# Performance work log

Measured on AMD Instinct MI355X. Metric: run time of the kernel, lower is better.

Reference implementation:

```python
import jax, jax.numpy as jnp
import numpy as np

N_NODES = 50000
N_HEDGES = 10000
NNZ_INC = 400000
NNZ_E = 80000
NNZ_V = 400000
VDIM = 128
EDIM = 128
OUT_VDIM = 128
OUT_EDIM = 128


def _spmm(rows, cols, vals, X, n_rows):
    # sparse COO [n_rows, n_cols] @ X  -> [n_rows, d]
    return jax.ops.segment_sum(vals[:, None] * X[cols], rows, num_segments=n_rows)


def setup_inputs() -> dict:
    key = jax.random.key(0)
    ks = jax.random.split(key, 20)
    inp = {
        "vfeat": jax.random.normal(ks[0], (N_NODES, VDIM), jnp.float32),
        "efeat": jax.random.normal(ks[1], (N_HEDGES, EDIM), jnp.float32),
        "invDV": jax.random.uniform(ks[2], (N_NODES,), jnp.float32),
        "invDE": jax.random.uniform(ks[3], (N_HEDGES,), jnp.float32),
        "inc_src": jax.random.randint(ks[4], (NNZ_INC,), 0, N_NODES, jnp.int32),
        "inc_dst": jax.random.randint(ks[5], (NNZ_INC,), 0, N_HEDGES, jnp.int32),
        "emat_rows": jax.random.randint(ks[6], (NNZ_E,), 0, N_HEDGES, jnp.int32),
        "emat_cols": jax.random.randint(ks[7], (NNZ_E,), 0, N_HEDGES, jnp.int32),
        "emat_vals": jax.random.normal(ks[8], (NNZ_E,), jnp.float32),
        "vmat_rows": jax.random.randint(ks[9], (NNZ_V,), 0, N_NODES, jnp.int32),
        "vmat_cols": jax.random.randint(ks[10], (NNZ_V,), 0, N_NODES, jnp.int32),
        "vmat_vals": jax.random.normal(ks[11], (NNZ_V,), jnp.float32),
        # parameters (torch Linear: y = x @ W.T + b)
        "Wv": jax.random.normal(ks[12], (OUT_VDIM, VDIM), jnp.float32) * 0.05,
        "We": jax.random.normal(ks[13], (OUT_EDIM, EDIM), jnp.float32) * 0.05,
        "psi1_W": jax.random.normal(ks[14], (VDIM, VDIM + EDIM), jnp.float32) * 0.05,
        "psi1_b": jnp.zeros((VDIM,), jnp.float32),
        "psi2_W": jax.random.normal(ks[15], (EDIM, OUT_VDIM + EDIM), jnp.float32) * 0.05,
        "psi2_b": jnp.zeros((EDIM,), jnp.float32),
    }
    return inp


def reference(vfeat, efeat, invDV, invDE, inc_src, inc_dst,
              emat_rows, emat_cols, emat_vals,
              vmat_rows, vmat_cols, vmat_vals,
              Wv, We, psi1_W, psi1_b, psi2_W, psi2_b):
    N = vfeat.shape[0]
    E = efeat.shape[0]
    # --- 'in' update_all with psi1: per-incidence concat -> linear -> *invDV[src] -> sum into hyperedge
    x = jnp.concatenate([vfeat[inc_src], efeat[inc_dst]], axis=1)  # [nnz, VDIM+EDIM]
    x = x @ psi1_W.T + psi1_b                                       # [nnz, VDIM]
    x = x * invDV[inc_src][:, None]
    A = jax.ops.segment_sum(x, inc_dst, num_segments=E)             # [E, VDIM]
    A = _spmm(emat_rows, emat_cols, emat_vals, A, E)
    _efeat = A + efeat
    # --- 'con' update_all: node gathers sum of incident hyperedge feats
    _vfeat = jax.ops.segment_sum(_efeat[inc_dst], inc_src, num_segments=N)
    vfeat_out = jax.nn.relu(_vfeat @ Wv.T)                           # [N, OUT_VDIM]
    # --- 'in' update_all with psi2 (dv = ones)
    x2 = jnp.concatenate([vfeat_out[inc_src], efeat[inc_dst]], axis=1)
    x2 = x2 @ psi2_W.T + psi2_b                                      # [nnz, EDIM]
    B = jax.ops.segment_sum(x2, inc_dst, num_segments=E) * invDE[:, None]
    # --- 'con' pass with efeat, then vMat spmm, then 'in' sum back to hyperedges
    _vfeat2 = jax.ops.segment_sum(efeat[inc_dst], inc_src, num_segments=N)
    _vfeat2 = _spmm(vmat_rows, vmat_cols, vmat_vals, _vfeat2, N)
    _efeat2 = jax.ops.segment_sum(_vfeat2[inc_src], inc_dst, num_segments=E)
    _efeat2 = _efeat2 + B
    efeat_out = jax.nn.relu(_efeat2 @ We.T)                          # [E, OUT_EDIM]
    return vfeat_out, efeat_out
```

## Files before the change

kernel.cpp:

```cpp
#include <hip/hip_runtime.h>

#define NN 50000
#define NE 10000
#define NNZ_INC 400000
#define NNZ_E 80000
#define NNZ_V 400000
#define D 128
#define KC 32

#define CAP_D 112
#define CAP_S 40
#define CAP_E 40
#define CAP_V 40

#define CSTR 16

#define GN_ 782
#define GE_ 157
#define G_HINC ((NNZ_INC + 255) / 256)
#define G_EV ((NNZ_E + NNZ_V + 255) / 256)
#define G_CVTN 6250
#define G_CVTE 1250
#define G_NR16 (NN / 16)
#define G_ER16 (NE / 16)

typedef unsigned short u16;
typedef unsigned int u32;

__device__ __forceinline__ u16 f2bf(float x) {
    unsigned u = __float_as_uint(x);
    unsigned r = u + 0x7fffu + ((u >> 16) & 1u);
    return (u16)(r >> 16);
}
__device__ __forceinline__ float bf2f(u16 h) {
    return __uint_as_float(((unsigned)h) << 16);
}

__device__ __forceinline__ void acc8(uint4 u, float acc[8]) {
    acc[0] += __uint_as_float(u.x << 16);
    acc[1] += __uint_as_float(u.x & 0xffff0000u);
    acc[2] += __uint_as_float(u.y << 16);
    acc[3] += __uint_as_float(u.y & 0xffff0000u);
    acc[4] += __uint_as_float(u.z << 16);
    acc[5] += __uint_as_float(u.z & 0xffff0000u);
    acc[6] += __uint_as_float(u.w << 16);
    acc[7] += __uint_as_float(u.w & 0xffff0000u);
}
__device__ __forceinline__ void fma8(uint4 u, float v, float acc[8]) {
    acc[0] = fmaf(v, __uint_as_float(u.x << 16), acc[0]);
    acc[1] = fmaf(v, __uint_as_float(u.x & 0xffff0000u), acc[1]);
    acc[2] = fmaf(v, __uint_as_float(u.y << 16), acc[2]);
    acc[3] = fmaf(v, __uint_as_float(u.y & 0xffff0000u), acc[3]);
    acc[4] = fmaf(v, __uint_as_float(u.z << 16), acc[4]);
    acc[5] = fmaf(v, __uint_as_float(u.z & 0xffff0000u), acc[5]);
    acc[6] = fmaf(v, __uint_as_float(u.w << 16), acc[6]);
    acc[7] = fmaf(v, __uint_as_float(u.w & 0xffff0000u), acc[7]);
}
__device__ __forceinline__ uint4 pack_bf8(const float acc[8]) {
    uint4 o;
    o.x = (u32)f2bf(acc[0]) | ((u32)f2bf(acc[1]) << 16);
    o.y = (u32)f2bf(acc[2]) | ((u32)f2bf(acc[3]) << 16);
    o.z = (u32)f2bf(acc[4]) | ((u32)f2bf(acc[5]) << 16);
    o.w = (u32)f2bf(acc[6]) | ((u32)f2bf(acc[7]) << 16);
    return o;
}

__device__ __forceinline__ void gemm_acc(
    int bx, const float* __restrict__ X, const float* __restrict__ W, int ldw,
    int M, float acc[8][4])
{
    __shared__ float XsT[KC][68];
    __shared__ float Ws[KC][132];
    const int tid = threadIdx.x;
    const int tx = tid & 31, ty = tid >> 5;
    const int row0 = bx * 64;
    const int c0 = tx * 4;
    const int r0 = ty * 8;

#pragma unroll
    for (int r = 0; r < 8; ++r)
#pragma unroll
        for (int c = 0; c < 4; ++c) acc[r][c] = 0.f;

    for (int kc = 0; kc < D; kc += KC) {
        __syncthreads();
#pragma unroll
        for (int it = 0; it < 2; ++it) {
            int l = tid + it * 256;
            int r = l >> 3, k4 = l & 7;
            float4 v = make_float4(0.f, 0.f, 0.f, 0.f);
            int row = row0 + r;
            if (row < M) v = ((const float4*)(X + (size_t)row * D + kc))[k4];
            int k = k4 * 4;
            XsT[k + 0][r] = v.x; XsT[k + 1][r] = v.y;
            XsT[k + 2][r] = v.z; XsT[k + 3][r] = v.w;
        }
#pragma unroll
        for (int it = 0; it < 4; ++it) {
            int l = tid + it * 256;
            int o = l >> 3, k4 = l & 7;
            float4 w = ((const float4*)(W + (size_t)o * ldw + kc))[k4];
            int k = k4 * 4;
            Ws[k + 0][o] = w.x; Ws[k + 1][o] = w.y;
            Ws[k + 2][o] = w.z; Ws[k + 3][o] = w.w;
        }
        __syncthreads();
#pragma unroll
        for (int k = 0; k < KC; ++k) {
            const float4 a0 = *(const float4*)&XsT[k][r0];
            const float4 a1 = *(const float4*)&XsT[k][r0 + 4];
            const float4 b  = *(const float4*)&Ws[k][c0];
            float av[8] = {a0.x, a0.y, a0.z, a0.w, a1.x, a1.y, a1.z, a1.w};
            float bv[4] = {b.x, b.y, b.z, b.w};
#pragma unroll
            for (int r = 0; r < 8; ++r)
#pragma unroll
                for (int c = 0; c < 4; ++c)
                    acc[r][c] = fmaf(av[r], bv[c], acc[r][c]);
        }
    }
}

__global__ __launch_bounds__(256) void mega0(
    const int* __restrict__ inc_src, const int* __restrict__ inc_dst,
    int* __restrict__ cnt_dst, int* __restrict__ cnt_src,
    u16* __restrict__ ell_d, u16* __restrict__ ell_s,
    const float* __restrict__ efeat, const float* __restrict__ vfeat,
    const float* __restrict__ invDV,
    const float* __restrict__ psi1_W, const float* __restrict__ psi1_b, float* __restrict__ PeP,
    const float* __restrict__ psi2_W, const float* __restrict__ psi2_b, float* __restrict__ QeP,
    u16* __restrict__ vfi_b, u16* __restrict__ efeat_b)
{
    int b = blockIdx.x;
    if (b < G_HINC) {
        int i = b * 256 + threadIdx.x;
        if (i < NNZ_INC) {
            int s = inc_src[i], d = inc_dst[i];
            int rd = atomicAdd(cnt_dst + (size_t)d * CSTR, 1);
            if (rd < CAP_D) ell_d[d * CAP_D + rd] = (u16)s;
            int rs = atomicAdd(cnt_src + (size_t)s * CSTR, 1);
            if (rs < CAP_S) ell_s[s * CAP_S + rs] = (u16)d;
        }
    } else if (b < G_HINC + 2 * GE_) {
        int lb = b - G_HINC;
        const float* Wp = (lb < GE_) ? psi1_W + D : psi2_W + D;
        const float* bp = (lb < GE_) ? psi1_b : psi2_b;
        float* outp     = (lb < GE_) ? PeP : QeP;
        int bx = (lb < GE_) ? lb : lb - GE_;
        float acc[8][4];
        gemm_acc(bx, efeat, Wp, 2 * D, NE, acc);
        int tx = threadIdx.x & 31, ty = threadIdx.x >> 5;
        float4 b4 = ((const float4*)bp)[tx];
#pragma unroll
        for (int r = 0; r < 8; ++r) {
            int row = bx * 64 + ty * 8 + r;
            if (row < NE) {
                float4 v = make_float4(acc[r][0] + b4.x, acc[r][1] + b4.y,
                                       acc[r][2] + b4.z, acc[r][3] + b4.w);
                ((float4*)(outp + (size_t)row * D))[tx] = v;
            }
        }
    } else if (b < G_HINC + 2 * GE_ + G_CVTN) {
        int i = ((b - G_HINC - 2 * GE_) * 256 + threadIdx.x) * 4;
        int row = i >> 7;
        float s = invDV[row];
        float4 v = *(const float4*)(vfeat + i);
        ushort4 u;
        u.x = f2bf(v.x * s); u.y = f2bf(v.y * s);
        u.z = f2bf(v.z * s); u.w = f2bf(v.w * s);
        *(ushort4*)(vfi_b + i) = u;
    } else {
        int i = ((b - G_HINC - 2 * GE_ - G_CVTN) * 256 + threadIdx.x) * 4;
        float4 v = *(const float4*)(efeat + i);
        ushort4 u;
        u.x = f2bf(v.x); u.y = f2bf(v.y); u.z = f2bf(v.z); u.w = f2bf(v.w);
        *(ushort4*)(efeat_b + i) = u;
    }
}

__device__ __forceinline__ void segsum_bf_ell16(int rb,
    const int* __restrict__ cnt, int cap, const u16* __restrict__ ell,
    const u16* __restrict__ Tb, u16* __restrict__ Yb, int R)
{
    int r = rb * 16 + (threadIdx.x >> 4);
    int q = threadIdx.x & 15;
    if (r >= R) return;
    int m = min(cnt[(size_t)r * CSTR], cap);
    const u16* lst = ell + (size_t)r * cap;
    float acc[8] = {0.f, 0.f, 0.f, 0.f, 0.f, 0.f, 0.f, 0.f};
    int j = 0;
    for (; j + 3 < m; j += 4) {
        ushort4 ix = *(const ushort4*)(lst + j);
        uint4 u0 = *(const uint4*)(Tb + (size_t)ix.x * D + q * 8);
        uint4 u1 = *(const uint4*)(Tb + (size_t)ix.y * D + q * 8);
        uint4 u2 = *(const uint4*)(Tb + (size_t)ix.z * D + q * 8);
        uint4 u3 = *(const uint4*)(Tb + (size_t)ix.w * D + q * 8);
        acc8(u0, acc); acc8(u1, acc); acc8(u2, acc); acc8(u3, acc);
    }
    for (; j < m; ++j) {
        uint4 u0 = *(const uint4*)(Tb + (size_t)lst[j] * D + q * 8);
        acc8(u0, acc);
    }
    ((uint4*)(Yb + (size_t)r * D))[q] = pack_bf8(acc);
}

__device__ __forceinline__ void segsum_f_ell16(int rb,
    const int* __restrict__ cnt, int cap, const u16* __restrict__ ell,
    const u16* __restrict__ Tb, float* __restrict__ Y, int R)
{
    int r = rb * 16 + (threadIdx.x >> 4);
    int q = threadIdx.x & 15;
    if (r >= R) return;
    int m = min(cnt[(size_t)r * CSTR], cap);
    const u16* lst = ell + (size_t)r * cap;
    float acc[8] = {0.f, 0.f, 0.f, 0.f, 0.f, 0.f, 0.f, 0.f};
    int j = 0;
    for (; j + 3 < m; j += 4) {
        ushort4 ix = *(const ushort4*)(lst + j);
        uint4 u0 = *(const uint4*)(Tb + (size_t)ix.x * D + q * 8);
        uint4 u1 = *(const uint4*)(Tb + (size_t)ix.y * D + q * 8);
        uint4 u2 = *(const uint4*)(Tb + (size_t)ix.z * D + q * 8);
        uint4 u3 = *(const uint4*)(Tb + (size_t)ix.w * D + q * 8);
        acc8(u0, acc); acc8(u1, acc); acc8(u2, acc); acc8(u3, acc);
    }
    for (; j < m; ++j) {
        uint4 u0 = *(const uint4*)(Tb + (size_t)lst[j] * D + q * 8);
        acc8(u0, acc);
    }
    float* yr = Y + (size_t)r * D;
    ((float4*)yr)[2 * q + 0] = make_float4(acc[0], acc[1], acc[2], acc[3]);
    ((float4*)yr)[2 * q + 1] = make_float4(acc[4], acc[5], acc[6], acc[7]);
}

__device__ __forceinline__ void spmm_bf_ell16(int rb,
    const int* __restrict__ cnt, int cap, const u32* __restrict__ ell,
    const u16* __restrict__ Xb, const float* __restrict__ addend,
    u16* __restrict__ Yb, int R)
{
    int r = rb * 16 + (threadIdx.x >> 4);
    int q = threadIdx.x & 15;
    if (r >= R) return;
    int m = min(cnt[(size_t)r * CSTR], cap);
    const u32* lst = ell + (size_t)r * cap;
    float acc[8];
    if (addend) {
        const float* ar = addend + (size_t)r * D;
        float4 lo = ((const float4*)ar)[2 * q + 0];
        float4 hi = ((const float4*)ar)[2 * q + 1];
        acc[0] = lo.x; acc[1] = lo.y; acc[2] = lo.z; acc[3] = lo.w;
        acc[4] = hi.x; acc[5] = hi.y; acc[6] = hi.z; acc[7] = hi.w;
    } else {
#pragma unroll
        for (int i = 0; i < 8; ++i) acc[i] = 0.f;
    }
    int j = 0;
    for (; j + 3 < m; j += 4) {
        uint4 e = *(const uint4*)(lst + j);
        uint4 x0 = *(const uint4*)(Xb + (size_t)(e.x >> 16) * D + q * 8);
        uint4 x1 = *(const uint4*)(Xb + (size_t)(e.y >> 16) * D + q * 8);
        uint4 x2 = *(const uint4*)(Xb + (size_t)(e.z >> 16) * D + q * 8);
        uint4 x3 = *(const uint4*)(Xb + (size_t)(e.w >> 16) * D + q * 8);
        fma8(x0, __uint_as_float(e.x << 16), acc);
        fma8(x1, __uint_as_float(e.y << 16), acc);
        fma8(x2, __uint_as_float(e.z << 16), acc);
        fma8(x3, __uint_as_float(e.w << 16), acc);
    }
    for (; j < m; ++j) {
        u32 e = lst[j];
        uint4 x = *(const uint4*)(Xb + (size_t)(e >> 16) * D + q * 8);
        fma8(x, __uint_as_float(e << 16), acc);
    }
    ((uint4*)(Yb + (size_t)r * D))[q] = pack_bf8(acc);
}

__global__ __launch_bounds__(256) void fusedA(
    const int* __restrict__ erows, const int* __restrict__ ecols,
    const float* __restrict__ evals, int* __restrict__ cnt_e, u32* __restrict__ ev_e,
    const int* __restrict__ vrows, const int* __restrict__ vcols,
    const float* __restrict__ vvals, int* __restrict__ cnt_v, u32* __restrict__ ev_v,
    const int* __restrict__ cnt_dst, const u16* __restrict__ ell_d,
    const float* __restrict__ invDV, const u16* __restrict__ vfi_b,
    float* __restrict__ sva, float* __restrict__ wsum,
    const int* __restrict__ cnt_src, const u16* __restrict__ ell_s,
    const u16* __restrict__ efeat_b, u16* __restrict__ vf2_b)
{
    int b = blockIdx.x;
    if (b < G_EV) {
        int i = b * 256 + threadIdx.x;
        if (i < NNZ_E) {
            int r = erows[i];
            int re = atomicAdd(cnt_e + (size_t)r * CSTR, 1);
            if (re < CAP_E)
                ev_e[r * CAP_E + re] = ((u32)ecols[i] << 16) | (u32)f2bf(evals[i]);
        } else if (i < NNZ_E + NNZ_V) {
            int j = i - NNZ_E;
            int r = vrows[j];
            int rv = atomicAdd(cnt_v + (size_t)r * CSTR, 1);
            if (rv < CAP_V)
                ev_v[r * CAP_V + rv] = ((u32)vcols[j] << 16) | (u32)f2bf(vvals[j]);
        }
    } else if (b < G_EV + G_ER16) {
        int e = (b - G_EV) * 16 + (threadIdx.x >> 4);
        int q = threadIdx.x & 15;
        if (e >= NE) return;
        int m = min(cnt_dst[(size_t)e * CSTR], CAP_D);
        const u16* lst = ell_d + (size_t)e * CAP_D;
        float acc[8] = {0.f, 0.f, 0.f, 0.f, 0.f, 0.f, 0.f, 0.f};
        float ws = 0.f;
        int j = 0;
        for (; j + 3 < m; j += 4) {
            ushort4 ix = *(const ushort4*)(lst + j);
            uint4 u0 = *(const uint4*)(vfi_b + (size_t)ix.x * D + q * 8);
            uint4 u1 = *(const uint4*)(vfi_b + (size_t)ix.y * D + q * 8);
            uint4 u2 = *(const uint4*)(vfi_b + (size_t)ix.z * D + q * 8);
            uint4 u3 = *(const uint4*)(vfi_b + (size_t)ix.w * D + q * 8);
            ws += (invDV[ix.x] + invDV[ix.y]) + (invDV[ix.z] + invDV[ix.w]);
            acc8(u0, acc); acc8(u1, acc); acc8(u2, acc); acc8(u3, acc);
        }
        for (; j < m; ++j) {
            int s = lst[j];
            uint4 u0 = *(const uint4*)(vfi_b + (size_t)s * D + q * 8);
            ws += invDV[s];
            acc8(u0, acc);
        }
        float* yr = sva + (size_t)e * D;
        ((float4*)yr)[2 * q + 0] = make_float4(acc[0], acc[1], acc[2], acc[3]);
        ((float4*)yr)[2 * q + 1] = make_float4(acc[4], acc[5], acc[6], acc[7]);
        if (q == 0) wsum[e] = ws;
    } else {
        segsum_bf_ell16(b - G_EV - G_ER16, cnt_src, CAP_S, ell_s, efeat_b, vf2_b, NN);
    }
}

__global__ __launch_bounds__(256) void gemmA_k(
    const float* __restrict__ sva, const float* __restrict__ psi1_W,
    const float* __restrict__ wsum, const float* __restrict__ PeP,
    u16* __restrict__ A_b)
{
    float acc[8][4];
    gemm_acc(blockIdx.x, sva, psi1_W, 2 * D, NE, acc);
    int tx = threadIdx.x & 31, ty = threadIdx.x >> 5;
#pragma unroll
    for (int r = 0; r < 8; ++r) {
        int row = blockIdx.x * 64 + ty * 8 + r;
        if (row < NE) {
            float ws = wsum[row];
            float4 pe = ((const float4*)(PeP + (size_t)row * D))[tx];
            ushort4 u;
            u.x = f2bf(fmaf(ws, pe.x, acc[r][0]));
            u.y = f2bf(fmaf(ws, pe.y, acc[r][1]));
            u.z = f2bf(fmaf(ws, pe.z, acc[r][2]));
            u.w = f2bf(fmaf(ws, pe.w, acc[r][3]));
            ((ushort4*)(A_b + (size_t)row * D))[tx] = u;
        }
    }
}

__global__ __launch_bounds__(256) void fusedB(
    const int* __restrict__ cnt_e, const u32* __restrict__ ev_e,
    const u16* __restrict__ A_b, const float* __restrict__ efeat, u16* __restrict__ A2_b,
    const int* __restrict__ cnt_v, const u32* __restrict__ ev_v,
    const u16* __restrict__ vf2_b, u16* __restrict__ vf2b_b)
{
    int b = blockIdx.x;
    if (b < G_ER16) spmm_bf_ell16(b, cnt_e, CAP_E, ev_e, A_b, efeat, A2_b, NE);
    else spmm_bf_ell16(b - G_ER16, cnt_v, CAP_V, ev_v, vf2_b, nullptr, vf2b_b, NN);
}

__global__ __launch_bounds__(256) void fusedD(
    const int* __restrict__ cnt_src, const u16* __restrict__ ell_s,
    const u16* __restrict__ A2_b, float* __restrict__ vf1,
    const int* __restrict__ cnt_dst, const u16* __restrict__ ell_d,
    const u16* __restrict__ vf2b_b, float* __restrict__ av)
{
    int b = blockIdx.x;
    if (b < G_NR16) segsum_f_ell16(b, cnt_src, CAP_S, ell_s, A2_b, vf1, NN);
    else segsum_f_ell16(b - G_NR16, cnt_dst, CAP_D, ell_d, vf2b_b, av, NE);
}

__global__ __launch_bounds__(256) void gemmC_k(
    const float* __restrict__ vf1, const float* __restrict__ Wv,
    float* __restrict__ out_v, u16* __restrict__ outv_b)
{
    float acc[8][4];
    gemm_acc(blockIdx.x, vf1, Wv, D, NN, acc);
    int tx = threadIdx.x & 31, ty = threadIdx.x >> 5;
#pragma unroll
    for (int r = 0; r < 8; ++r) {
        int row = blockIdx.x * 64 + ty * 8 + r;
        if (row < NN) {
            float4 v = make_float4(fmaxf(acc[r][0], 0.f), fmaxf(acc[r][1], 0.f),
                                   fmaxf(acc[r][2], 0.f), fmaxf(acc[r][3], 0.f));
            ((float4*)(out_v + (size_t)row * D))[tx] = v;
            ushort4 u;
            u.x = f2bf(v.x); u.y = f2bf(v.y); u.z = f2bf(v.z); u.w = f2bf(v.w);
            ((ushort4*)(outv_b + (size_t)row * D))[tx] = u;
        }
    }
}

__global__ __launch_bounds__(256) void gather_sv(
    const int* __restrict__ cnt_dst, const u16* __restrict__ ell_d,
    const u16* __restrict__ outv_b, float* __restrict__ sv)
{
    segsum_f_ell16(blockIdx.x, cnt_dst, CAP_D, ell_d, outv_b, sv, NE);
}

__global__ __launch_bounds__(256) void gemmBE_k(
    const float* __restrict__ sv, const float* __restrict__ psi2_W,
    const int* __restrict__ cnt_dst, const float* __restrict__ QeP,
    const float* __restrict__ invDE, const float* __restrict__ av,
    const float* __restrict__ We, float* __restrict__ out_e)
{
    __shared__ float T[D][68];
    float acc[8][4];
    gemm_acc(blockIdx.x, sv, psi2_W, 2 * D, NE, acc);
    const int tx = threadIdx.x & 31, ty = threadIdx.x >> 5;
    const int bx = blockIdx.x;
#pragma unroll
    for (int r = 0; r < 8; ++r) {
        int row = bx * 64 + ty * 8 + r;
        float deg = 0.f, ide = 0.f;
        float4 qe = make_float4(0.f, 0.f, 0.f, 0.f);
        float4 a  = make_float4(0.f, 0.f, 0.f, 0.f);
        if (row < NE) {
            deg = (float)cnt_dst[(size_t)row * CSTR];
            ide = invDE[row];
            qe = ((const float4*)(QeP + (size_t)row * D))[tx];
            a  = ((const float4*)(av  + (size_t)row * D))[tx];
        }
        int lr = ty * 8 + r;
        T[tx * 4 + 0][lr] = fmaf(deg, qe.x, acc[r][0]) * ide + a.x;
        T[tx * 4 + 1][lr] = fmaf(deg, qe.y, acc[r][1]) * ide + a.y;
        T[tx * 4 + 2][lr] = fmaf(deg, qe.z, acc[r][2]) * ide + a.z;
        T[tx * 4 + 3][lr] = fmaf(deg, qe.w, acc[r][3]) * ide + a.w;
    }
    __shared__ float Ws2[KC][132];
    float acc2[8][4];
#pragma unroll
    for (int r = 0; r < 8; ++r)
#pragma unroll
        for (int c = 0; c < 4; ++c) acc2[r][c] = 0.f;
    const int c0 = tx * 4, r0 = ty * 8;
    for (int kc = 0; kc < D; kc += KC) {
        __syncthreads();
#pragma unroll
        for (int it = 0; it < 4; ++it) {
            int l = threadIdx.x + it * 256;
            int o = l >> 3, k4 = l & 7;
            float4 w = ((const float4*)(We + (size_t)o * D + kc))[k4];
            int k = k4 * 4;
            Ws2[k + 0][o] = w.x; Ws2[k + 1][o] = w.y;
            Ws2[k + 2][o] = w.z; Ws2[k + 3][o] = w.w;
        }
        __syncthreads();
#pragma unroll
        for (int k = 0; k < KC; ++k) {
            const float4 a0 = *(const float4*)&T[kc + k][r0];
            const float4 a1 = *(const float4*)&T[kc + k][r0 + 4];
            const float4 bb = *(const float4*)&Ws2[k][c0];
            float avv[8] = {a0.x, a0.y, a0.z, a0.w, a1.x, a1.y, a1.z, a1.w};
            float bv[4] = {bb.x, bb.y, bb.z, bb.w};
#pragma unroll
            for (int r = 0; r < 8; ++r)
#pragma unroll
                for (int c = 0; c < 4; ++c)
                    acc2[r][c] = fmaf(avv[r], bv[c], acc2[r][c]);
        }
    }
#pragma unroll
    for (int r = 0; r < 8; ++r) {
        int row = bx * 64 + ty * 8 + r;
        if (row < NE) {
            float4 v = make_float4(fmaxf(acc2[r][0], 0.f), fmaxf(acc2[r][1], 0.f),
                                   fmaxf(acc2[r][2], 0.f), fmaxf(acc2[r][3], 0.f));
            ((float4*)(out_e + (size_t)row * D))[tx] = v;
        }
    }
}

extern "C" void kernel_launch(void* const* d_in, const int* in_sizes, int n_in,
                              void* d_out, int out_size, void* d_ws, size_t ws_size,
                              hipStream_t stream)
{
    (void)in_sizes; (void)n_in; (void)out_size; (void)ws_size;
    const float* vfeat     = (const float*)d_in[0];
    const float* efeat     = (const float*)d_in[1];
    const float* invDV     = (const float*)d_in[2];
    const float* invDE     = (const float*)d_in[3];
    const int*   inc_src   = (const int*)d_in[4];
    const int*   inc_dst   = (const int*)d_in[5];
    const int*   emat_rows = (const int*)d_in[6];
    const int*   emat_cols = (const int*)d_in[7];
    const float* emat_vals = (const float*)d_in[8];
    const int*   vmat_rows = (const int*)d_in[9];
    const int*   vmat_cols = (const int*)d_in[10];
    const float* vmat_vals = (const float*)d_in[11];
    const float* Wv        = (const float*)d_in[12];
    const float* We        = (const float*)d_in[13];
    const float* psi1_W    = (const float*)d_in[14];
    const float* psi1_b    = (const float*)d_in[15];
    const float* psi2_W    = (const float*)d_in[16];
    const float* psi2_b    = (const float*)d_in[17];

    const size_t ND = (size_t)NN * D;
    const size_t ED = (size_t)NE * D;

    char* p = (char*)d_ws;
    auto alloc = [&](size_t bytes) {
        size_t a = (size_t)p; a = (a + 255) & ~(size_t)255;
        p = (char*)a; void* r = (void*)p; p += bytes; return r;
    };
    float* PeP   = (float*)alloc(ED * 4);
    float* QeP   = (float*)alloc(ED * 4);
    float* vf1   = (float*)alloc(ND * 4);
    float* av    = (float*)alloc(ED * 4);
    float* svbuf = (float*)alloc(ED * 4);
    float* wsum  = (float*)alloc((size_t)NE * 4);
    u16* vfi_b   = (u16*)alloc(ND * 2);
    u16* outv_b  = (u16*)alloc(ND * 2);
    u16* vf2_b   = (u16*)alloc(ND * 2);
    u16* vf2b_b  = (u16*)alloc(ND * 2);
    u16* efeat_b = (u16*)alloc(ED * 2);
    u16* A_b     = (u16*)alloc(ED * 2);
    u16* A2_b    = (u16*)alloc(ED * 2);
    int* cnt_dst = (int*)alloc((size_t)(2 * NE + 2 * NN) * CSTR * 4);
    int* cnt_src = cnt_dst + (size_t)NE * CSTR;
    int* cnt_e   = cnt_src + (size_t)NN * CSTR;
    int* cnt_v   = cnt_e + (size_t)NE * CSTR;
    u16* ell_d   = (u16*)alloc((size_t)NE * CAP_D * 2);
    u16* ell_s   = (u16*)alloc((size_t)NN * CAP_S * 2);
    u32* ev_e    = (u32*)alloc((size_t)NE * CAP_E * 4);
    u32* ev_v    = (u32*)alloc((size_t)NN * CAP_V * 4);

    float* out_v = (float*)d_out;
    float* out_e = out_v + ND;

    dim3 b256(256);

    hipMemsetAsync(cnt_dst, 0, (size_t)(2 * NE + 2 * NN) * CSTR * sizeof(int), stream);
    mega0<<<G_HINC + 2 * GE_ + G_CVTN + G_CVTE, b256, 0, stream>>>(
        inc_src, inc_dst, cnt_dst, cnt_src, ell_d, ell_s,
        efeat, vfeat, invDV,
        psi1_W, psi1_b, PeP, psi2_W, psi2_b, QeP, vfi_b, efeat_b);
    fusedA<<<G_EV + G_ER16 + G_NR16, b256, 0, stream>>>(
        emat_rows, emat_cols, emat_vals, cnt_e, ev_e,
        vmat_rows, vmat_cols, vmat_vals, cnt_v, ev_v,
        cnt_dst, ell_d, invDV, vfi_b, svbuf, wsum,
        cnt_src, ell_s, efeat_b, vf2_b);
    gemmA_k<<<GE_, b256, 0, stream>>>(svbuf, psi1_W, wsum, PeP, A_b);
    fusedB<<<G_ER16 + G_NR16, b256, 0, stream>>>(
        cnt_e, ev_e, A_b, efeat, A2_b,
        cnt_v, ev_v, vf2_b, vf2b_b);
    fusedD<<<G_NR16 + G_ER16, b256, 0, stream>>>(
        cnt_src, ell_s, A2_b, vf1,
        cnt_dst, ell_d, vf2b_b, av);
    gemmC_k<<<GN_, b256, 0, stream>>>(vf1, Wv, out_v, outv_b);
    gather_sv<<<G_ER16, b256, 0, stream>>>(cnt_dst, ell_d, outv_b, svbuf);
    gemmBE_k<<<GE_, b256, 0, stream>>>(svbuf, psi2_W, cnt_dst, QeP, invDE, av, We, out_e);
}
```

Measured before the change: 365.4 us.

## Pack degree counters densely and move efeat GEMM blocks into second fused kernel

Removes the 16-int stride padding on the atomic degree counters, so the counters sit densely and the memset shrinks. This risks more atomic contention on shared cache lines. It also moves the efeat @ psi W GEMM blocks (PeP/QeP) out of the first launch, which holds the incidence atomics, and into the second fused launch. The aim is to balance work between the two launches and shorten the atomic-bound first kernel.

After: 365.1 us. About the same (-0.1%).

```diff
diff --git a/kernel.cpp b/kernel.cpp
--- a/kernel.cpp
+++ b/kernel.cpp
@@ -12,8 +12,6 @@
 #define CAP_S 40
 #define CAP_E 40
 #define CAP_V 40
-
-#define CSTR 16
 
 #define GN_ 782
 #define GE_ 157
@@ -127,8 +125,6 @@
     u16* __restrict__ ell_d, u16* __restrict__ ell_s,
     const float* __restrict__ efeat, const float* __restrict__ vfeat,
     const float* __restrict__ invDV,
-    const float* __restrict__ psi1_W, const float* __restrict__ psi1_b, float* __restrict__ PeP,
-    const float* __restrict__ psi2_W, const float* __restrict__ psi2_b, float* __restrict__ QeP,
     u16* __restrict__ vfi_b, u16* __restrict__ efeat_b)
 {
     int b = blockIdx.x;
@@ -136,32 +132,13 @@
         int i = b * 256 + threadIdx.x;
         if (i < NNZ_INC) {
             int s = inc_src[i], d = inc_dst[i];
-            int rd = atomicAdd(cnt_dst + (size_t)d * CSTR, 1);
+            int rd = atomicAdd(cnt_dst + d, 1);
             if (rd < CAP_D) ell_d[d * CAP_D + rd] = (u16)s;
-            int rs = atomicAdd(cnt_src + (size_t)s * CSTR, 1);
+            int rs = atomicAdd(cnt_src + s, 1);
             if (rs < CAP_S) ell_s[s * CAP_S + rs] = (u16)d;
         }
-    } else if (b < G_HINC + 2 * GE_) {
-        int lb = b - G_HINC;
-        const float* Wp = (lb < GE_) ? psi1_W + D : psi2_W + D;
-        const float* bp = (lb < GE_) ? psi1_b : psi2_b;
-        float* outp     = (lb < GE_) ? PeP : QeP;
-        int bx = (lb < GE_) ? lb : lb - GE_;
-        float acc[8][4];
-        gemm_acc(bx, efeat, Wp, 2 * D, NE, acc);
-        int tx = threadIdx.x & 31, ty = threadIdx.x >> 5;
-        float4 b4 = ((const float4*)bp)[tx];
-#pragma unroll
-        for (int r = 0; r < 8; ++r) {
-            int row = bx * 64 + ty * 8 + r;
-            if (row < NE) {
-                float4 v = make_float4(acc[r][0] + b4.x, acc[r][1] + b4.y,
-                                       acc[r][2] + b4.z, acc[r][3] + b4.w);
-                ((float4*)(outp + (size_t)row * D))[tx] = v;
-            }
-        }
-    } else if (b < G_HINC + 2 * GE_ + G_CVTN) {
-        int i = ((b - G_HINC - 2 * GE_) * 256 + threadIdx.x) * 4;
+    } else if (b < G_HINC + G_CVTN) {
+        int i = ((b - G_HINC) * 256 + threadIdx.x) * 4;
         int row = i >> 7;
         float s = invDV[row];
         float4 v = *(const float4*)(vfeat + i);
@@ -170,7 +147,7 @@
         u.z = f2bf(v.z * s); u.w = f2bf(v.w * s);
         *(ushort4*)(vfi_b + i) = u;
     } else {
-        int i = ((b - G_HINC - 2 * GE_ - G_CVTN) * 256 + threadIdx.x) * 4;
+        int i = ((b - G_HINC - G_CVTN) * 256 + threadIdx.x) * 4;
         float4 v = *(const float4*)(efeat + i);
         ushort4 u;
         u.x = f2bf(v.x); u.y = f2bf(v.y); u.z = f2bf(v.z); u.w = f2bf(v.w);
@@ -185,7 +162,7 @@
     int r = rb * 16 + (threadIdx.x >> 4);
     int q = threadIdx.x & 15;
     if (r >= R) return;
-    int m = min(cnt[(size_t)r * CSTR], cap);
+    int m = min(cnt[r], cap);
     const u16* lst = ell + (size_t)r * cap;
     float acc[8] = {0.f, 0.f, 0.f, 0.f, 0.f, 0.f, 0.f, 0.f};
     int j = 0;
@@ -211,7 +188,7 @@
     int r = rb * 16 + (threadIdx.x >> 4);
     int q = threadIdx.x & 15;
     if (r >= R) return;
-    int m = min(cnt[(size_t)r * CSTR], cap);
+    int m = min(cnt[r], cap);
     const u16* lst = ell + (size_t)r * cap;
     float acc[8] = {0.f, 0.f, 0.f, 0.f, 0.f, 0.f, 0.f, 0.f};
     int j = 0;
@@ -240,7 +217,7 @@
     int r = rb * 16 + (threadIdx.x >> 4);
     int q = threadIdx.x & 15;
     if (r >= R) return;
-    int m = min(cnt[(size_t)r * CSTR], cap);
+    int m = min(cnt[r], cap);
     const u32* lst = ell + (size_t)r * cap;
     float acc[8];
     if (addend) {
@@ -278,6 +255,9 @@
     const float* __restrict__ evals, int* __restrict__ cnt_e, u32* __restrict__ ev_e,
     const int* __restrict__ vrows, const int* __restrict__ vcols,
     const float* __restrict__ vvals, int* __restrict__ cnt_v, u32* __restrict__ ev_v,
+    const float* __restrict__ efeat,
+    const float* __restrict__ psi1_W, const float* __restrict__ psi1_b, float* __restrict__ PeP,
+    const float* __restrict__ psi2_W, const float* __restrict__ psi2_b, float* __restrict__ QeP,
     const int* __restrict__ cnt_dst, const u16* __restrict__ ell_d,
     const float* __restrict__ invDV, const u16* __restrict__ vfi_b,
     float* __restrict__ sva, float* __restrict__ wsum,
@@ -289,21 +269,40 @@
         int i = b * 256 + threadIdx.x;
         if (i < NNZ_E) {
             int r = erows[i];
-            int re = atomicAdd(cnt_e + (size_t)r * CSTR, 1);
+            int re = atomicAdd(cnt_e + r, 1);
             if (re < CAP_E)
                 ev_e[r * CAP_E + re] = ((u32)ecols[i] << 16) | (u32)f2bf(evals[i]);
         } else if (i < NNZ_E + NNZ_V) {
             int j = i - NNZ_E;
             int r = vrows[j];
-            int rv = atomicAdd(cnt_v + (size_t)r * CSTR, 1);
+            int rv = atomicAdd(cnt_v + r, 1);
             if (rv < CAP_V)
                 ev_v[r * CAP_V + rv] = ((u32)vcols[j] << 16) | (u32)f2bf(vvals[j]);
         }
-    } else if (b < G_EV + G_ER16) {
-        int e = (b - G_EV) * 16 + (threadIdx.x >> 4);
+    } else if (b < G_EV + 2 * GE_) {
+        int lb = b - G_EV;
+        const float* Wp = (lb < GE_) ? psi1_W + D : psi2_W + D;
+        const float* bp = (lb < GE_) ? psi1_b : psi2_b;
+        float* outp     = (lb < GE_) ? PeP : QeP;
+        int bx = (lb < GE_) ? lb : lb - GE_;
+        float acc[8][4];
+        gemm_acc(bx, efeat, Wp, 2 * D, NE, acc);
+        int tx = threadIdx.x & 31, ty = threadIdx.x >> 5;
+        float4 b4 = ((const float4*)bp)[tx];
+#pragma unroll
+        for (int r = 0; r < 8; ++r) {
+            int row = bx * 64 + ty * 8 + r;
+            if (row < NE) {
+                float4 v = make_float4(acc[r][0] + b4.x, acc[r][1] + b4.y,
+                                       acc[r][2] + b4.z, acc[r][3] + b4.w);
+                ((float4*)(outp + (size_t)row * D))[tx] = v;
+            }
+        }
+    } else if (b < G_EV + 2 * GE_ + G_ER16) {
+        int e = (b - G_EV - 2 * GE_) * 16 + (threadIdx.x >> 4);
         int q = threadIdx.x & 15;
         if (e >= NE) return;
-        int m = min(cnt_dst[(size_t)e * CSTR], CAP_D);
+        int m = min(cnt_dst[e], CAP_D);
         const u16* lst = ell_d + (size_t)e * CAP_D;
         float acc[8] = {0.f, 0.f, 0.f, 0.f, 0.f, 0.f, 0.f, 0.f};
         float ws = 0.f;
@@ -328,7 +327,7 @@
         ((float4*)yr)[2 * q + 1] = make_float4(acc[4], acc[5], acc[6], acc[7]);
         if (q == 0) wsum[e] = ws;
     } else {
-        segsum_bf_ell16(b - G_EV - G_ER16, cnt_src, CAP_S, ell_s, efeat_b, vf2_b, NN);
+        segsum_bf_ell16(b - G_EV - 2 * GE_ - G_ER16, cnt_src, CAP_S, ell_s, efeat_b, vf2_b, NN);
     }
 }
 
@@ -424,7 +423,7 @@
         float4 qe = make_float4(0.f, 0.f, 0.f, 0.f);
         float4 a  = make_float4(0.f, 0.f, 0.f, 0.f);
         if (row < NE) {
-            deg = (float)cnt_dst[(size_t)row * CSTR];
+            deg = (float)cnt_dst[row];
             ide = invDE[row];
             qe = ((const float4*)(QeP + (size_t)row * D))[tx];
             a  = ((const float4*)(av  + (size_t)row * D))[tx];
@@ -524,10 +523,10 @@
     u16* efeat_b = (u16*)alloc(ED * 2);
     u16* A_b     = (u16*)alloc(ED * 2);
     u16* A2_b    = (u16*)alloc(ED * 2);
-    int* cnt_dst = (int*)alloc((size_t)(2 * NE + 2 * NN) * CSTR * 4);
-    int* cnt_src = cnt_dst + (size_t)NE * CSTR;
-    int* cnt_e   = cnt_src + (size_t)NN * CSTR;
-    int* cnt_v   = cnt_e + (size_t)NE * CSTR;
+    int* cnt_dst = (int*)alloc((size_t)(2 * NE + 2 * NN) * 4);
+    int* cnt_src = cnt_dst + NE;
+    int* cnt_e   = cnt_src + NN;
+    int* cnt_v   = cnt_e + NE;
     u16* ell_d   = (u16*)alloc((size_t)NE * CAP_D * 2);
     u16* ell_s   = (u16*)alloc((size_t)NN * CAP_S * 2);
     u32* ev_e    = (u32*)alloc((size_t)NE * CAP_E * 4);
@@ -538,14 +537,14 @@
 
     dim3 b256(256);
 
-    hipMemsetAsync(cnt_dst, 0, (size_t)(2 * NE + 2 * NN) * CSTR * sizeof(int), stream);
-    mega0<<<G_HINC + 2 * GE_ + G_CVTN + G_CVTE, b256, 0, stream>>>(
+    hipMemsetAsync(cnt_dst, 0, (size_t)(2 * NE + 2 * NN) * sizeof(int), stream);
+    mega0<<<G_HINC + G_CVTN + G_CVTE, b256, 0, stream>>>(
         inc_src, inc_dst, cnt_dst, cnt_src, ell_d, ell_s,
-        efeat, vfeat, invDV,
-        psi1_W, psi1_b, PeP, psi2_W, psi2_b, QeP, vfi_b, efeat_b);
-    fusedA<<<G_EV + G_ER16 + G_NR16, b256, 0, stream>>>(
+        efeat, vfeat, invDV, vfi_b, efeat_b);
+    fusedA<<<G_EV + 2 * GE_ + G_ER16 + G_NR16, b256, 0, stream>>>(
         emat_rows, emat_cols, emat_vals, cnt_e, ev_e,
         vmat_rows, vmat_cols, vmat_vals, cnt_v, ev_v,
+        efeat, psi1_W, psi1_b, PeP, psi2_W, psi2_b, QeP,
         cnt_dst, ell_d, invDV, vfi_b, svbuf, wsum,
         cnt_src, ell_s, efeat_b, vf2_b);
     gemmA_k<<<GE_, b256, 0, stream>>>(svbuf, psi1_W, wsum, PeP, A_b);
```
